# Kernel optimization log

Hardware: AMD Instinct MI355X
Metric: run time of the kernel (lower is better)

Reference implementation:

```python
import jax, jax.numpy as jnp
import numpy as np

N = 50000
E = 800000
G = 2500  # number of graphs


def setup_inputs() -> dict:
    key = jax.random.key(0)
    ks = jax.random.split(key, 10)
    x = jax.random.normal(ks[0], (N, 128), dtype=jnp.float32)
    edge_index = jax.random.randint(ks[1], (2, E), 0, N, dtype=jnp.int64)
    batch = jnp.sort(jax.random.randint(ks[2], (N,), 0, G, dtype=jnp.int64))
    def lin(k, fan_in, shape):
        return jax.random.normal(k, shape, dtype=jnp.float32) / np.sqrt(fan_in)
    return {
        'x': x, 'edge_index': edge_index, 'batch': batch,
        'W1': lin(ks[3], 128, (128, 64)), 'b1': jnp.zeros((64,), jnp.float32),
        'W2': lin(ks[4], 64, (64, 64)),  'b2': jnp.zeros((64,), jnp.float32),
        'W3': lin(ks[5], 64, (64, 64)),  'b3': jnp.zeros((64,), jnp.float32),
        'Wp1': lin(ks[6], 64, (64, 64)), 'bp1': jnp.zeros((64,), jnp.float32),
        'Wp2': lin(ks[7], 64, (64, 32)), 'bp2': jnp.zeros((32,), jnp.float32),
    }


def _gcn_norm(edge_index, n_nodes):
    # PyG GCNConv default: add self-loops, symmetric normalization
    loops = jnp.arange(n_nodes, dtype=edge_index.dtype)
    src = jnp.concatenate([edge_index[0], loops])
    dst = jnp.concatenate([edge_index[1], loops])
    deg = jax.ops.segment_sum(jnp.ones_like(dst, dtype=jnp.float32), dst,
                              num_segments=n_nodes)
    dis = jnp.where(deg > 0, jax.lax.rsqrt(deg), 0.0)
    norm = dis[src] * dis[dst]  # [E + N]
    return src, dst, norm


def _gcn_conv(x, W, b, src, dst, norm, n_nodes):
    h = x @ W                                   # transform first (small dim)
    m = h[src] * norm[:, None]                  # gather + scale
    out = jax.ops.segment_sum(m, dst, num_segments=n_nodes)  # scatter-add
    return out + b


def reference(x, edge_index, batch, W1, b1, W2, b2, W3, b3, Wp1, bp1, Wp2, bp2):
    n_nodes = x.shape[0]
    src, dst, norm = _gcn_norm(edge_index, n_nodes)
    x1 = jax.nn.relu(_gcn_conv(x, W1, b1, src, dst, norm, n_nodes))
    x2 = jax.nn.relu(_gcn_conv(x1, W2, b2, src, dst, norm, n_nodes))
    x3 = jax.nn.relu(_gcn_conv(x2, W3, b3, src, dst, norm, n_nodes))
    h = x1 + x2 + x3
    # global_mean_pool
    sums = jax.ops.segment_sum(h, batch, num_segments=G)
    counts = jax.ops.segment_sum(jnp.ones((n_nodes,), jnp.float32), batch,
                                 num_segments=G)
    pooled = sums / jnp.maximum(counts, 1.0)[:, None]
    z = jax.nn.relu(pooled @ Wp1 + bp1) @ Wp2 + bp2
    return z
```

## Files before the change

kernel.cpp:

```cpp
#include <hip/hip_runtime.h>
#include <math.h>


typedef short short8 __attribute__((ext_vector_type(8)));
typedef float f32x4 __attribute__((ext_vector_type(4)));

__device__ inline float bf2f(unsigned short h) {
    return __uint_as_float((unsigned)h << 16);
}
__device__ inline unsigned short f2bf(float f) {
    unsigned u = __float_as_uint(f);
    return (unsigned short)((u + (0x7FFFu + ((u >> 16) & 1u))) >> 16);
}
__device__ inline void bh8f(short8 u, float4& a, float4& b) {
    a.x = bf2f((unsigned short)u[0]); a.y = bf2f((unsigned short)u[1]);
    a.z = bf2f((unsigned short)u[2]); a.w = bf2f((unsigned short)u[3]);
    b.x = bf2f((unsigned short)u[4]); b.y = bf2f((unsigned short)u[5]);
    b.z = bf2f((unsigned short)u[6]); b.w = bf2f((unsigned short)u[7]);
}
__device__ inline float4 f4add(float4 a, float4 acc) {
    acc.x += a.x; acc.y += a.y; acc.z += a.z; acc.w += a.w;
    return acc;
}

template <int K>
__global__ __launch_bounds__(256) void k_hist_gemm(const int* __restrict__ dst,
                                                   int* __restrict__ hist, int E, int chunk,
                                                   const float* __restrict__ X,
                                                   const float* __restrict__ W,
                                                   unsigned short* __restrict__ H, int n) {
    __shared__ int hh[256];
    __shared__ short wt[64 * K];
    int t = threadIdx.x;
    if (blockIdx.x < 256) {
        hh[t] = 0;
        __syncthreads();
        int e0 = blockIdx.x * chunk;
        int e1 = min(e0 + chunk, E);
        for (int e = e0 + t; e < e1; e += 256) atomicAdd(&hh[dst[e] >> 8], 1);
        __syncthreads();
        hist[blockIdx.x * 256 + t] = hh[t];
        return;
    }
    for (int idx = t; idx < 64 * K; idx += 256) {
        int k = idx >> 6, ch = idx & 63;
        wt[ch * K + k] = (short)f2bf(W[idx]);
    }
    __syncthreads();
    int wave = t >> 6, lane = t & 63;
    int q = lane >> 4, l = lane & 15;
    int tile = (blockIdx.x - 256) * 4 + wave;
    if (tile * 16 >= n) return;
    int node = tile * 16 + l;
    short8 afr[4][K / 32];
#pragma unroll
    for (int mb = 0; mb < 4; mb++)
#pragma unroll
        for (int s = 0; s < K / 32; s++)
            afr[mb][s] = *(const short8*)(wt + (mb * 16 + l) * K + s * 32 + q * 8);
    f32x4 acc[4] = {};
    const float* xr = X + (size_t)node * K + q * 8;
#pragma unroll
    for (int s = 0; s < K / 32; s++) {
        float4 xa = *(const float4*)(xr + s * 32);
        float4 xb = *(const float4*)(xr + s * 32 + 4);
        short8 bfr;
        bfr[0] = (short)f2bf(xa.x); bfr[1] = (short)f2bf(xa.y);
        bfr[2] = (short)f2bf(xa.z); bfr[3] = (short)f2bf(xa.w);
        bfr[4] = (short)f2bf(xb.x); bfr[5] = (short)f2bf(xb.y);
        bfr[6] = (short)f2bf(xb.z); bfr[7] = (short)f2bf(xb.w);
#pragma unroll
        for (int mb = 0; mb < 4; mb++)
            acc[mb] = __builtin_amdgcn_mfma_f32_16x16x32_bf16(afr[mb][s], bfr, acc[mb], 0, 0, 0);
    }
#pragma unroll
    for (int mb = 0; mb < 4; mb++) {
        ushort4 u;
        u.x = f2bf(acc[mb][0]); u.y = f2bf(acc[mb][1]);
        u.z = f2bf(acc[mb][2]); u.w = f2bf(acc[mb][3]);
        ((ushort4*)H)[(size_t)node * 16 + mb * 4 + q] = u;
    }
}

__global__ void kA_colscan(const int* __restrict__ hist, int* __restrict__ cursorA,
                           int* __restrict__ tot) {
    __shared__ int s[256];
    int t = threadIdx.x;
    int k = blockIdx.x;
    int v = hist[t * 256 + k];
    s[t] = v;
    __syncthreads();
    for (int st = 1; st < 256; st <<= 1) {
        int u = s[t];
        if (t >= st) u += s[t - st];
        __syncthreads();
        s[t] = u;
        __syncthreads();
    }
    cursorA[t * 256 + k] = s[t] - v;
    if (t == 255) tot[k] = s[255];
}

__global__ void kA_scatter(const int* __restrict__ src, const int* __restrict__ dst,
                           const int* __restrict__ cursorA, const int* __restrict__ tot,
                           unsigned* __restrict__ ebuf, int E, int chunk) {
    __shared__ int s[256];
    __shared__ int cur[256];
    int t = threadIdx.x;
    s[t] = tot[t];
    __syncthreads();
    for (int st = 1; st < 256; st <<= 1) {
        int u = s[t];
        if (t >= st) u += s[t - st];
        __syncthreads();
        s[t] = u;
        __syncthreads();
    }
    int bstart = (t == 0) ? 0 : s[t - 1];
    cur[t] = cursorA[blockIdx.x * 256 + t] + bstart;
    __syncthreads();
    int e0 = blockIdx.x * chunk;
    int e1 = min(e0 + chunk, E);
    for (int e = e0 + t; e < e1; e += 256) {
        int d = dst[e];
        int p = atomicAdd(&cur[d >> 8], 1);
        ebuf[p] = ((unsigned)(d & 255) << 24) | (unsigned)src[e];
    }
}

__global__ void kB(const unsigned* __restrict__ ebuf, const int* __restrict__ tot,
                   float* __restrict__ dis, int* __restrict__ offsP,
                   unsigned* __restrict__ col, unsigned short* __restrict__ Hb,
                   unsigned short* __restrict__ Hb2, int* __restrict__ perm,
                   int N, int ZR) {
    __shared__ int s[256];
    __shared__ int h[256];
    __shared__ int cur[256];
    __shared__ float sdis[256];
    __shared__ int lh[128];
    __shared__ int ls[128];
    int t = threadIdx.x;
    int k = blockIdx.x;
    s[t] = tot[t];
    if (t < 128) lh[t] = 0;
    __syncthreads();
    for (int st = 1; st < 256; st <<= 1) {
        int u = s[t];
        if (t >= st) u += s[t - st];
        __syncthreads();
        s[t] = u;
        __syncthreads();
    }
    int lo = (k == 0) ? 0 : s[k - 1];
    int hi = s[k];
    int padbase = ((lo + 3) & ~3) + 768 * k;
    h[t] = 0;
    __syncthreads();
    for (int p = lo + t; p < hi; p += 256) atomicAdd(&h[ebuf[p] >> 24], 1);
    __syncthreads();
    int c = h[t];
    int cp = (c + 3) & ~3;
    int node = k * 256 + t;
    float dn = rsqrtf((float)(c + 1));
    sdis[t] = dn;
    if (node < N) dis[node] = dn;
    int bin = cp >> 2;
    if (bin > 127) bin = 127;
    bin = 127 - bin;
    int rk = 0;
    if (node < N) rk = atomicAdd(&lh[bin], 1);
    s[t] = cp;
    __syncthreads();
    for (int st = 1; st < 256; st <<= 1) {
        int u = s[t];
        if (t >= st) u += s[t - st];
        __syncthreads();
        s[t] = u;
        __syncthreads();
    }
    int start = padbase + s[t] - cp;
    if (node < N) offsP[node] = (start << 9) | cp;
    cur[t] = start;
    if (t < 128) ls[t] = lh[t];
    __syncthreads();
    for (int st = 1; st < 128; st <<= 1) {
        int u = 0;
        if (t < 128) { u = ls[t]; if (t >= st) u += ls[t - st]; }
        __syncthreads();
        if (t < 128) ls[t] = u;
        __syncthreads();
    }
    if (node < N) perm[k * 256 + ls[bin] - lh[bin] + rk] = node;
    for (int p = lo + t; p < hi; p += 256) {
        unsigned e = ebuf[p];
        int q = atomicAdd(&cur[e >> 24], 1);
        col[q] = e & 0x00FFFFFFu;
    }
    __syncthreads();
    if (node < N) {
        int end = start + cp;
        for (int q = cur[t]; q < end; q++) col[q] = (unsigned)ZR;
    }
    for (int idx = t; idx < 2048; idx += 256) {
        int nl = idx >> 3, cs = idx & 7;
        int nd = k * 256 + nl;
        if (nd >= N) continue;
        float d2 = sdis[nl];
        short8 v = ((const short8*)Hb)[(size_t)nd * 8 + cs];
        float4 a, b;
        bh8f(v, a, b);
        short8 o;
        o[0] = (short)f2bf(a.x * d2); o[1] = (short)f2bf(a.y * d2);
        o[2] = (short)f2bf(a.z * d2); o[3] = (short)f2bf(a.w * d2);
        o[4] = (short)f2bf(b.x * d2); o[5] = (short)f2bf(b.y * d2);
        o[6] = (short)f2bf(b.z * d2); o[7] = (short)f2bf(b.w * d2);
        ((short8*)Hb)[(size_t)nd * 8 + cs] = o;
    }
    if (k == 0) {
        if (t < 32) ((unsigned*)Hb)[(size_t)ZR * 32 + t] = 0u;
        else if (t < 64) ((unsigned*)Hb2)[(size_t)ZR * 32 + (t - 32)] = 0u;
    }
}

__global__ __launch_bounds__(256) void k_aggemm(const unsigned short* __restrict__ H,
                                                const unsigned* __restrict__ col,
                                                const int* __restrict__ offsP,
                                                const float* __restrict__ dis,
                                                const float* __restrict__ bias,
                                                const float* __restrict__ W,
                                                const int* __restrict__ perm,
                                                unsigned short* __restrict__ Xout,
                                                unsigned short* __restrict__ Hout, int n) {
    __shared__ short wt[64 * 64];
    __shared__ short vbuf[64 * 72];
    int t = threadIdx.x;
    for (int idx = t; idx < 64 * 64; idx += 256) {
        int k = idx >> 6, ch = idx & 63;
        wt[ch * 64 + k] = (short)f2bf(W[idx]);
    }
    const short8* Hs = (const short8*)H;
    int base = blockIdx.x * 64;
    int cs = t & 7;
    const float4* bias4 = (const float4*)bias;
    float4 bb0 = bias4[cs * 2];
    float4 bb1 = bias4[cs * 2 + 1];
#pragma unroll
    for (int r = 0; r < 2; r++) {
        int nl = r * 32 + (t >> 3);
        int slot = base + nl;
        if (slot < n) {
            int node = perm[slot];
            float dn = dis[node];
            float4 acc0, acc1;
            bh8f(Hs[(size_t)node * 8 + cs], acc0, acc1);
            int po = offsP[node];
            int p = po >> 9, hiP = p + (po & 511);
            for (; p + 8 <= hiP; p += 8) {
                uint4 ea = *(const uint4*)(col + p);
                uint4 eb = *(const uint4*)(col + p + 4);
                short8 g0 = Hs[(size_t)ea.x * 8 + cs];
                short8 g1 = Hs[(size_t)ea.y * 8 + cs];
                short8 g2 = Hs[(size_t)ea.z * 8 + cs];
                short8 g3 = Hs[(size_t)ea.w * 8 + cs];
                short8 g4 = Hs[(size_t)eb.x * 8 + cs];
                short8 g5 = Hs[(size_t)eb.y * 8 + cs];
                short8 g6 = Hs[(size_t)eb.z * 8 + cs];
                short8 g7 = Hs[(size_t)eb.w * 8 + cs];
                float4 a, b;
                bh8f(g0, a, b); acc0 = f4add(a, acc0); acc1 = f4add(b, acc1);
                bh8f(g1, a, b); acc0 = f4add(a, acc0); acc1 = f4add(b, acc1);
                bh8f(g2, a, b); acc0 = f4add(a, acc0); acc1 = f4add(b, acc1);
                bh8f(g3, a, b); acc0 = f4add(a, acc0); acc1 = f4add(b, acc1);
                bh8f(g4, a, b); acc0 = f4add(a, acc0); acc1 = f4add(b, acc1);
                bh8f(g5, a, b); acc0 = f4add(a, acc0); acc1 = f4add(b, acc1);
                bh8f(g6, a, b); acc0 = f4add(a, acc0); acc1 = f4add(b, acc1);
                bh8f(g7, a, b); acc0 = f4add(a, acc0); acc1 = f4add(b, acc1);
            }
            if (p < hiP) {
                uint4 e4 = *(const uint4*)(col + p);
                short8 g0 = Hs[(size_t)e4.x * 8 + cs];
                short8 g1 = Hs[(size_t)e4.y * 8 + cs];
                short8 g2 = Hs[(size_t)e4.z * 8 + cs];
                short8 g3 = Hs[(size_t)e4.w * 8 + cs];
                float4 a, b;
                bh8f(g0, a, b); acc0 = f4add(a, acc0); acc1 = f4add(b, acc1);
                bh8f(g1, a, b); acc0 = f4add(a, acc0); acc1 = f4add(b, acc1);
                bh8f(g2, a, b); acc0 = f4add(a, acc0); acc1 = f4add(b, acc1);
                bh8f(g3, a, b); acc0 = f4add(a, acc0); acc1 = f4add(b, acc1);
            }
            float4 v0, v1;
            v0.x = fmaxf(acc0.x * dn + bb0.x, 0.f);
            v0.y = fmaxf(acc0.y * dn + bb0.y, 0.f);
            v0.z = fmaxf(acc0.z * dn + bb0.z, 0.f);
            v0.w = fmaxf(acc0.w * dn + bb0.w, 0.f);
            v1.x = fmaxf(acc1.x * dn + bb1.x, 0.f);
            v1.y = fmaxf(acc1.y * dn + bb1.y, 0.f);
            v1.z = fmaxf(acc1.z * dn + bb1.z, 0.f);
            v1.w = fmaxf(acc1.w * dn + bb1.w, 0.f);
            short8 o;
            o[0] = (short)f2bf(v0.x); o[1] = (short)f2bf(v0.y);
            o[2] = (short)f2bf(v0.z); o[3] = (short)f2bf(v0.w);
            o[4] = (short)f2bf(v1.x); o[5] = (short)f2bf(v1.y);
            o[6] = (short)f2bf(v1.z); o[7] = (short)f2bf(v1.w);
            ((short8*)Xout)[(size_t)node * 8 + cs] = o;
            *(short8*)(vbuf + nl * 72 + cs * 8) = o;
        }
    }
    __syncthreads();
    int wave = t >> 6, lane = t & 63;
    int q = lane >> 4, l = lane & 15;
    if (base + wave * 16 >= n) return;
    int node = perm[base + wave * 16 + l];
    float dn2 = dis[node];
    short8 afr[4][2];
#pragma unroll
    for (int mb = 0; mb < 4; mb++)
#pragma unroll
        for (int s = 0; s < 2; s++)
            afr[mb][s] = *(const short8*)(wt + (mb * 16 + l) * 64 + s * 32 + q * 8);
    f32x4 acc[4] = {};
#pragma unroll
    for (int s = 0; s < 2; s++) {
        short8 bfr = *(const short8*)(vbuf + (wave * 16 + l) * 72 + s * 32 + q * 8);
#pragma unroll
        for (int mb = 0; mb < 4; mb++)
            acc[mb] = __builtin_amdgcn_mfma_f32_16x16x32_bf16(afr[mb][s], bfr, acc[mb], 0, 0, 0);
    }
#pragma unroll
    for (int mb = 0; mb < 4; mb++) {
        ushort4 u;
        u.x = f2bf(acc[mb][0] * dn2); u.y = f2bf(acc[mb][1] * dn2);
        u.z = f2bf(acc[mb][2] * dn2); u.w = f2bf(acc[mb][3] * dn2);
        ((ushort4*)Hout)[(size_t)node * 16 + mb * 4 + q] = u;
    }
}

__global__ void k_agg3(const unsigned short* __restrict__ H, const unsigned* __restrict__ col,
                       const int* __restrict__ offsP, const float* __restrict__ dis,
                       const float* __restrict__ bias,
                       const unsigned short* __restrict__ add1,
                       const unsigned short* __restrict__ add2,
                       const int* __restrict__ perm,
                       float* __restrict__ OutS, int n) {
    int t = threadIdx.x;
    int slot = blockIdx.x * 32 + (t >> 3);
    if (slot >= n) return;
    int node = perm[slot];
    int lane = t & 7;
    const short8* Hs = (const short8*)H;
    float dn = dis[node];
    float4 acc0, acc1;
    bh8f(Hs[(size_t)node * 8 + lane], acc0, acc1);
    int po = offsP[node];
    int p = po >> 9, hiP = p + (po & 511);
    for (; p + 8 <= hiP; p += 8) {
        uint4 ea = *(const uint4*)(col + p);
        uint4 eb = *(const uint4*)(col + p + 4);
        short8 g0 = Hs[(size_t)ea.x * 8 + lane];
        short8 g1 = Hs[(size_t)ea.y * 8 + lane];
        short8 g2 = Hs[(size_t)ea.z * 8 + lane];
        short8 g3 = Hs[(size_t)ea.w * 8 + lane];
        short8 g4 = Hs[(size_t)eb.x * 8 + lane];
        short8 g5 = Hs[(size_t)eb.y * 8 + lane];
        short8 g6 = Hs[(size_t)eb.z * 8 + lane];
        short8 g7 = Hs[(size_t)eb.w * 8 + lane];
        float4 a, b;
        bh8f(g0, a, b); acc0 = f4add(a, acc0); acc1 = f4add(b, acc1);
        bh8f(g1, a, b); acc0 = f4add(a, acc0); acc1 = f4add(b, acc1);
        bh8f(g2, a, b); acc0 = f4add(a, acc0); acc1 = f4add(b, acc1);
        bh8f(g3, a, b); acc0 = f4add(a, acc0); acc1 = f4add(b, acc1);
        bh8f(g4, a, b); acc0 = f4add(a, acc0); acc1 = f4add(b, acc1);
        bh8f(g5, a, b); acc0 = f4add(a, acc0); acc1 = f4add(b, acc1);
        bh8f(g6, a, b); acc0 = f4add(a, acc0); acc1 = f4add(b, acc1);
        bh8f(g7, a, b); acc0 = f4add(a, acc0); acc1 = f4add(b, acc1);
    }
    if (p < hiP) {
        uint4 e4 = *(const uint4*)(col + p);
        short8 g0 = Hs[(size_t)e4.x * 8 + lane];
        short8 g1 = Hs[(size_t)e4.y * 8 + lane];
        short8 g2 = Hs[(size_t)e4.z * 8 + lane];
        short8 g3 = Hs[(size_t)e4.w * 8 + lane];
        float4 a, b;
        bh8f(g0, a, b); acc0 = f4add(a, acc0); acc1 = f4add(b, acc1);
        bh8f(g1, a, b); acc0 = f4add(a, acc0); acc1 = f4add(b, acc1);
        bh8f(g2, a, b); acc0 = f4add(a, acc0); acc1 = f4add(b, acc1);
        bh8f(g3, a, b); acc0 = f4add(a, acc0); acc1 = f4add(b, acc1);
    }
    const float4* bias4 = (const float4*)bias;
    float4 bb0 = bias4[lane * 2];
    float4 bb1 = bias4[lane * 2 + 1];
    float4 v0, v1;
    v0.x = fmaxf(acc0.x * dn + bb0.x, 0.f);
    v0.y = fmaxf(acc0.y * dn + bb0.y, 0.f);
    v0.z = fmaxf(acc0.z * dn + bb0.z, 0.f);
    v0.w = fmaxf(acc0.w * dn + bb0.w, 0.f);
    v1.x = fmaxf(acc1.x * dn + bb1.x, 0.f);
    v1.y = fmaxf(acc1.y * dn + bb1.y, 0.f);
    v1.z = fmaxf(acc1.z * dn + bb1.z, 0.f);
    v1.w = fmaxf(acc1.w * dn + bb1.w, 0.f);
    size_t slotR = (size_t)node * 8 + lane;
    float4 a10, a11, a20, a21;
    bh8f(((const short8*)add1)[slotR], a10, a11);
    bh8f(((const short8*)add2)[slotR], a20, a21);
    v0.x += a10.x + a20.x; v0.y += a10.y + a20.y;
    v0.z += a10.z + a20.z; v0.w += a10.w + a20.w;
    v1.x += a11.x + a21.x; v1.y += a11.y + a21.y;
    v1.z += a11.z + a21.z; v1.w += a11.w + a21.w;
    float4* S4 = (float4*)OutS;
    size_t oi = (size_t)node * 16 + (size_t)lane * 2;
    S4[oi] = v0;
    S4[oi + 1] = v1;
}

__global__ void k_poolhead(const float* __restrict__ S, const int* __restrict__ batch,
                           const float* __restrict__ Wp1, const float* __restrict__ bp1,
                           const float* __restrict__ Wp2, const float* __restrict__ bp2,
                           float* __restrict__ out, int n, int G) {
    int g = blockIdx.x;
    int j = threadIdx.x;
    int a = 0, b = n;
    while (a < b) { int m = (a + b) >> 1; if (batch[m] < g) a = m + 1; else b = m; }
    int beg = a;
    b = n;
    while (a < b) { int m = (a + b) >> 1; if (batch[m] < g + 1) a = m + 1; else b = m; }
    int end = a;
    float sum = 0.f;
    int i = beg;
    for (; i + 2 <= end; i += 2)
        sum += S[(size_t)i * 64 + j] + S[(size_t)(i + 1) * 64 + j];
    if (i < end) sum += S[(size_t)i * 64 + j];
    float cnt = (float)(end - beg);
    float p = sum / fmaxf(cnt, 1.f);
    __shared__ float ps[64];
    __shared__ float ts[64];
    ps[j] = p;
    __syncthreads();
    float t1 = bp1[j];
#pragma unroll 8
    for (int k = 0; k < 64; k++) t1 += ps[k] * Wp1[k * 64 + j];
    t1 = fmaxf(t1, 0.f);
    ts[j] = t1;
    __syncthreads();
    if (j < 32) {
        float o = bp2[j];
#pragma unroll 8
        for (int k = 0; k < 64; k++) o += ts[k] * Wp2[k * 32 + j];
        out[(size_t)g * 32 + j] = o;
    }
}

extern "C" void kernel_launch(void* const* d_in, const int* in_sizes, int n_in,
                              void* d_out, int out_size, void* d_ws, size_t ws_size,
                              hipStream_t stream) {
    const float* x   = (const float*)d_in[0];
    const int*   ei  = (const int*)d_in[1];
    const int*   bat = (const int*)d_in[2];
    const float* W1  = (const float*)d_in[3];
    const float* b1  = (const float*)d_in[4];
    const float* W2  = (const float*)d_in[5];
    const float* b2  = (const float*)d_in[6];
    const float* W3  = (const float*)d_in[7];
    const float* b3  = (const float*)d_in[8];
    const float* Wp1 = (const float*)d_in[9];
    const float* bp1 = (const float*)d_in[10];
    const float* Wp2 = (const float*)d_in[11];
    const float* bp2 = (const float*)d_in[12];

    int N = in_sizes[0] / 128;
    int E = in_sizes[1] / 2;
    int G = out_size / 32;
    const int* src = ei;
    const int* dst = ei + E;

    char* w = (char*)d_ws;
    auto alloc = [&](size_t bytes) -> void* {
        void* p = (void*)w;
        w += (bytes + 255) & ~(size_t)255;
        return p;
    };
    int NB = (N + 255) / 256;
    int ZR = N;
    int*            offsP   = (int*)alloc((size_t)N * 4);
    unsigned*       col     = (unsigned*)alloc(((size_t)E + 3 * (size_t)N + 2048) * 4);
    float*          dis     = (float*)alloc((size_t)N * 4);
    int*            hist    = (int*)alloc((size_t)256 * 256 * 4);
    int*            cursorA = (int*)alloc((size_t)256 * 256 * 4);
    int*            tot     = (int*)alloc((size_t)256 * 4);
    unsigned*       ebuf    = (unsigned*)alloc((size_t)E * 4);
    int*            perm    = (int*)alloc((size_t)(NB * 256) * 4);
    unsigned short* Hb      = (unsigned short*)alloc(((size_t)N + 16) * 64 * 2);
    unsigned short* Hb2     = (unsigned short*)alloc(((size_t)N + 16) * 64 * 2);
    unsigned short* X1      = (unsigned short*)alloc((size_t)N * 64 * 2);
    unsigned short* X2      = (unsigned short*)alloc((size_t)N * 64 * 2);
    float*          S       = (float*)alloc((size_t)N * 64 * 4);

    int chunk = (E + 255) / 256;
    int ggemm = ((N >> 4) + 3) / 4;
    int gfuse = (N + 63) / 64;
    int gagg  = (N + 31) / 32;

    k_hist_gemm<128><<<256 + ggemm, 256, 0, stream>>>(dst, hist, E, chunk, x, W1, Hb, N);
    kA_colscan<<<256, 256, 0, stream>>>(hist, cursorA, tot);
    kA_scatter<<<256, 256, 0, stream>>>(src, dst, cursorA, tot, ebuf, E, chunk);
    kB<<<NB, 256, 0, stream>>>(ebuf, tot, dis, offsP, col, Hb, Hb2, perm, N, ZR);

    k_aggemm<<<gfuse, 256, 0, stream>>>(Hb, col, offsP, dis, b1, W2, perm, X1, Hb2, N);
    k_aggemm<<<gfuse, 256, 0, stream>>>(Hb2, col, offsP, dis, b2, W3, perm, X2, Hb, N);
    k_agg3<<<gagg, 256, 0, stream>>>(Hb, col, offsP, dis, b3, X1, X2, perm, S, N);

    k_poolhead<<<G, 64, 0, stream>>>(S, bat, Wp1, bp1, Wp2, bp2, (float*)d_out, N, G);
}
```

Measured before the change: 221.2 us.

## Drop degree-sorted node permutation and use 32-node blocks in fused aggregate-GEMM

Removes the per-block degree-binning permutation built in kB (histogram, scan, perm writes) and the perm indirection in the aggregation kernels, so nodes are processed in natural order. k_aggemm now handles 32 nodes per 256-thread block instead of 64, which doubles the grid, and only two waves run the MFMA projection. The gains are less scan and sync work in kB, one fewer indirect load per node, and more blocks for the scheduler. The cost is that per-wave degree balancing is lost, so waves can diverge on uneven neighbor counts, and half the waves sit idle during the matrix step.

After: 215.5 us. -2.6%, faster.

```diff
diff --git a/kernel.cpp b/kernel.cpp
--- a/kernel.cpp
+++ b/kernel.cpp
@@ -131,18 +131,14 @@
 __global__ void kB(const unsigned* __restrict__ ebuf, const int* __restrict__ tot,
                    float* __restrict__ dis, int* __restrict__ offsP,
                    unsigned* __restrict__ col, unsigned short* __restrict__ Hb,
-                   unsigned short* __restrict__ Hb2, int* __restrict__ perm,
-                   int N, int ZR) {
+                   unsigned short* __restrict__ Hb2, int N, int ZR) {
     __shared__ int s[256];
     __shared__ int h[256];
     __shared__ int cur[256];
     __shared__ float sdis[256];
-    __shared__ int lh[128];
-    __shared__ int ls[128];
     int t = threadIdx.x;
     int k = blockIdx.x;
     s[t] = tot[t];
-    if (t < 128) lh[t] = 0;
     __syncthreads();
     for (int st = 1; st < 256; st <<= 1) {
         int u = s[t];
@@ -164,11 +160,6 @@
     float dn = rsqrtf((float)(c + 1));
     sdis[t] = dn;
     if (node < N) dis[node] = dn;
-    int bin = cp >> 2;
-    if (bin > 127) bin = 127;
-    bin = 127 - bin;
-    int rk = 0;
-    if (node < N) rk = atomicAdd(&lh[bin], 1);
     s[t] = cp;
     __syncthreads();
     for (int st = 1; st < 256; st <<= 1) {
@@ -181,16 +172,7 @@
     int start = padbase + s[t] - cp;
     if (node < N) offsP[node] = (start << 9) | cp;
     cur[t] = start;
-    if (t < 128) ls[t] = lh[t];
-    __syncthreads();
-    for (int st = 1; st < 128; st <<= 1) {
-        int u = 0;
-        if (t < 128) { u = ls[t]; if (t >= st) u += ls[t - st]; }
-        __syncthreads();
-        if (t < 128) ls[t] = u;
-        __syncthreads();
-    }
-    if (node < N) perm[k * 256 + ls[bin] - lh[bin] + rk] = node;
+    __syncthreads();
     for (int p = lo + t; p < hi; p += 256) {
         unsigned e = ebuf[p];
         int q = atomicAdd(&cur[e >> 24], 1);
@@ -228,90 +210,86 @@
                                                 const float* __restrict__ dis,
                                                 const float* __restrict__ bias,
                                                 const float* __restrict__ W,
-                                                const int* __restrict__ perm,
                                                 unsigned short* __restrict__ Xout,
                                                 unsigned short* __restrict__ Hout, int n) {
     __shared__ short wt[64 * 64];
-    __shared__ short vbuf[64 * 72];
+    __shared__ short vbuf[32 * 72];
     int t = threadIdx.x;
     for (int idx = t; idx < 64 * 64; idx += 256) {
         int k = idx >> 6, ch = idx & 63;
         wt[ch * 64 + k] = (short)f2bf(W[idx]);
     }
     const short8* Hs = (const short8*)H;
-    int base = blockIdx.x * 64;
+    int base = blockIdx.x * 32;
     int cs = t & 7;
+    int nl = t >> 3;
+    int node = base + nl;
     const float4* bias4 = (const float4*)bias;
     float4 bb0 = bias4[cs * 2];
     float4 bb1 = bias4[cs * 2 + 1];
-#pragma unroll
-    for (int r = 0; r < 2; r++) {
-        int nl = r * 32 + (t >> 3);
-        int slot = base + nl;
-        if (slot < n) {
-            int node = perm[slot];
-            float dn = dis[node];
-            float4 acc0, acc1;
-            bh8f(Hs[(size_t)node * 8 + cs], acc0, acc1);
-            int po = offsP[node];
-            int p = po >> 9, hiP = p + (po & 511);
-            for (; p + 8 <= hiP; p += 8) {
-                uint4 ea = *(const uint4*)(col + p);
-                uint4 eb = *(const uint4*)(col + p + 4);
-                short8 g0 = Hs[(size_t)ea.x * 8 + cs];
-                short8 g1 = Hs[(size_t)ea.y * 8 + cs];
-                short8 g2 = Hs[(size_t)ea.z * 8 + cs];
-                short8 g3 = Hs[(size_t)ea.w * 8 + cs];
-                short8 g4 = Hs[(size_t)eb.x * 8 + cs];
-                short8 g5 = Hs[(size_t)eb.y * 8 + cs];
-                short8 g6 = Hs[(size_t)eb.z * 8 + cs];
-                short8 g7 = Hs[(size_t)eb.w * 8 + cs];
-                float4 a, b;
-                bh8f(g0, a, b); acc0 = f4add(a, acc0); acc1 = f4add(b, acc1);
-                bh8f(g1, a, b); acc0 = f4add(a, acc0); acc1 = f4add(b, acc1);
-                bh8f(g2, a, b); acc0 = f4add(a, acc0); acc1 = f4add(b, acc1);
-                bh8f(g3, a, b); acc0 = f4add(a, acc0); acc1 = f4add(b, acc1);
-                bh8f(g4, a, b); acc0 = f4add(a, acc0); acc1 = f4add(b, acc1);
-                bh8f(g5, a, b); acc0 = f4add(a, acc0); acc1 = f4add(b, acc1);
-                bh8f(g6, a, b); acc0 = f4add(a, acc0); acc1 = f4add(b, acc1);
-                bh8f(g7, a, b); acc0 = f4add(a, acc0); acc1 = f4add(b, acc1);
-            }
-            if (p < hiP) {
-                uint4 e4 = *(const uint4*)(col + p);
-                short8 g0 = Hs[(size_t)e4.x * 8 + cs];
-                short8 g1 = Hs[(size_t)e4.y * 8 + cs];
-                short8 g2 = Hs[(size_t)e4.z * 8 + cs];
-                short8 g3 = Hs[(size_t)e4.w * 8 + cs];
-                float4 a, b;
-                bh8f(g0, a, b); acc0 = f4add(a, acc0); acc1 = f4add(b, acc1);
-                bh8f(g1, a, b); acc0 = f4add(a, acc0); acc1 = f4add(b, acc1);
-                bh8f(g2, a, b); acc0 = f4add(a, acc0); acc1 = f4add(b, acc1);
-                bh8f(g3, a, b); acc0 = f4add(a, acc0); acc1 = f4add(b, acc1);
-            }
-            float4 v0, v1;
-            v0.x = fmaxf(acc0.x * dn + bb0.x, 0.f);
-            v0.y = fmaxf(acc0.y * dn + bb0.y, 0.f);
-            v0.z = fmaxf(acc0.z * dn + bb0.z, 0.f);
-            v0.w = fmaxf(acc0.w * dn + bb0.w, 0.f);
-            v1.x = fmaxf(acc1.x * dn + bb1.x, 0.f);
-            v1.y = fmaxf(acc1.y * dn + bb1.y, 0.f);
-            v1.z = fmaxf(acc1.z * dn + bb1.z, 0.f);
-            v1.w = fmaxf(acc1.w * dn + bb1.w, 0.f);
-            short8 o;
-            o[0] = (short)f2bf(v0.x); o[1] = (short)f2bf(v0.y);
-            o[2] = (short)f2bf(v0.z); o[3] = (short)f2bf(v0.w);
-            o[4] = (short)f2bf(v1.x); o[5] = (short)f2bf(v1.y);
-            o[6] = (short)f2bf(v1.z); o[7] = (short)f2bf(v1.w);
-            ((short8*)Xout)[(size_t)node * 8 + cs] = o;
-            *(short8*)(vbuf + nl * 72 + cs * 8) = o;
+    if (node < n) {
+        float dn = dis[node];
+        float4 acc0, acc1;
+        bh8f(Hs[(size_t)node * 8 + cs], acc0, acc1);
+        int po = offsP[node];
+        int p = po >> 9, hiP = p + (po & 511);
+        for (; p + 8 <= hiP; p += 8) {
+            uint4 ea = *(const uint4*)(col + p);
+            uint4 eb = *(const uint4*)(col + p + 4);
+            short8 g0 = Hs[(size_t)ea.x * 8 + cs];
+            short8 g1 = Hs[(size_t)ea.y * 8 + cs];
+            short8 g2 = Hs[(size_t)ea.z * 8 + cs];
+            short8 g3 = Hs[(size_t)ea.w * 8 + cs];
+            short8 g4 = Hs[(size_t)eb.x * 8 + cs];
+            short8 g5 = Hs[(size_t)eb.y * 8 + cs];
+            short8 g6 = Hs[(size_t)eb.z * 8 + cs];
+            short8 g7 = Hs[(size_t)eb.w * 8 + cs];
+            float4 a, b;
+            bh8f(g0, a, b); acc0 = f4add(a, acc0); acc1 = f4add(b, acc1);
+            bh8f(g1, a, b); acc0 = f4add(a, acc0); acc1 = f4add(b, acc1);
+            bh8f(g2, a, b); acc0 = f4add(a, acc0); acc1 = f4add(b, acc1);
+            bh8f(g3, a, b); acc0 = f4add(a, acc0); acc1 = f4add(b, acc1);
+            bh8f(g4, a, b); acc0 = f4add(a, acc0); acc1 = f4add(b, acc1);
+            bh8f(g5, a, b); acc0 = f4add(a, acc0); acc1 = f4add(b, acc1);
+            bh8f(g6, a, b); acc0 = f4add(a, acc0); acc1 = f4add(b, acc1);
+            bh8f(g7, a, b); acc0 = f4add(a, acc0); acc1 = f4add(b, acc1);
         }
+        if (p < hiP) {
+            uint4 e4 = *(const uint4*)(col + p);
+            short8 g0 = Hs[(size_t)e4.x * 8 + cs];
+            short8 g1 = Hs[(size_t)e4.y * 8 + cs];
+            short8 g2 = Hs[(size_t)e4.z * 8 + cs];
+            short8 g3 = Hs[(size_t)e4.w * 8 + cs];
+            float4 a, b;
+            bh8f(g0, a, b); acc0 = f4add(a, acc0); acc1 = f4add(b, acc1);
+            bh8f(g1, a, b); acc0 = f4add(a, acc0); acc1 = f4add(b, acc1);
+            bh8f(g2, a, b); acc0 = f4add(a, acc0); acc1 = f4add(b, acc1);
+            bh8f(g3, a, b); acc0 = f4add(a, acc0); acc1 = f4add(b, acc1);
+        }
+        float4 v0, v1;
+        v0.x = fmaxf(acc0.x * dn + bb0.x, 0.f);
+        v0.y = fmaxf(acc0.y * dn + bb0.y, 0.f);
+        v0.z = fmaxf(acc0.z * dn + bb0.z, 0.f);
+        v0.w = fmaxf(acc0.w * dn + bb0.w, 0.f);
+        v1.x = fmaxf(acc1.x * dn + bb1.x, 0.f);
+        v1.y = fmaxf(acc1.y * dn + bb1.y, 0.f);
+        v1.z = fmaxf(acc1.z * dn + bb1.z, 0.f);
+        v1.w = fmaxf(acc1.w * dn + bb1.w, 0.f);
+        short8 o;
+        o[0] = (short)f2bf(v0.x); o[1] = (short)f2bf(v0.y);
+        o[2] = (short)f2bf(v0.z); o[3] = (short)f2bf(v0.w);
+        o[4] = (short)f2bf(v1.x); o[5] = (short)f2bf(v1.y);
+        o[6] = (short)f2bf(v1.z); o[7] = (short)f2bf(v1.w);
+        ((short8*)Xout)[(size_t)node * 8 + cs] = o;
+        *(short8*)(vbuf + nl * 72 + cs * 8) = o;
     }
     __syncthreads();
     int wave = t >> 6, lane = t & 63;
+    if (wave >= 2) return;
     int q = lane >> 4, l = lane & 15;
     if (base + wave * 16 >= n) return;
-    int node = perm[base + wave * 16 + l];
-    float dn2 = dis[node];
+    int mnode = base + wave * 16 + l;
+    float dn2 = dis[mnode];
     short8 afr[4][2];
 #pragma unroll
     for (int mb = 0; mb < 4; mb++)
@@ -331,7 +309,7 @@
         ushort4 u;
         u.x = f2bf(acc[mb][0] * dn2); u.y = f2bf(acc[mb][1] * dn2);
         u.z = f2bf(acc[mb][2] * dn2); u.w = f2bf(acc[mb][3] * dn2);
-        ((ushort4*)Hout)[(size_t)node * 16 + mb * 4 + q] = u;
+        ((ushort4*)Hout)[(size_t)mnode * 16 + mb * 4 + q] = u;
     }
 }
 
@@ -340,12 +318,10 @@
                        const float* __restrict__ bias,
                        const unsigned short* __restrict__ add1,
                        const unsigned short* __restrict__ add2,
-                       const int* __restrict__ perm,
                        float* __restrict__ OutS, int n) {
     int t = threadIdx.x;
-    int slot = blockIdx.x * 32 + (t >> 3);
-    if (slot >= n) return;
-    int node = perm[slot];
+    int node = blockIdx.x * 32 + (t >> 3);
+    if (node >= n) return;
     int lane = t & 7;
     const short8* Hs = (const short8*)H;
     float dn = dis[node];
@@ -398,10 +374,10 @@
     v1.y = fmaxf(acc1.y * dn + bb1.y, 0.f);
     v1.z = fmaxf(acc1.z * dn + bb1.z, 0.f);
     v1.w = fmaxf(acc1.w * dn + bb1.w, 0.f);
-    size_t slotR = (size_t)node * 8 + lane;
+    size_t slot = (size_t)node * 8 + lane;
     float4 a10, a11, a20, a21;
-    bh8f(((const short8*)add1)[slotR], a10, a11);
-    bh8f(((const short8*)add2)[slotR], a20, a21);
+    bh8f(((const short8*)add1)[slot], a10, a11);
+    bh8f(((const short8*)add2)[slot], a20, a21);
     v0.x += a10.x + a20.x; v0.y += a10.y + a20.y;
     v0.z += a10.z + a20.z; v0.w += a10.w + a20.w;
     v1.x += a11.x + a21.x; v1.y += a11.y + a21.y;
@@ -487,7 +463,6 @@
     int*            cursorA = (int*)alloc((size_t)256 * 256 * 4);
     int*            tot     = (int*)alloc((size_t)256 * 4);
     unsigned*       ebuf    = (unsigned*)alloc((size_t)E * 4);
-    int*            perm    = (int*)alloc((size_t)(NB * 256) * 4);
     unsigned short* Hb      = (unsigned short*)alloc(((size_t)N + 16) * 64 * 2);
     unsigned short* Hb2     = (unsigned short*)alloc(((size_t)N + 16) * 64 * 2);
     unsigned short* X1      = (unsigned short*)alloc((size_t)N * 64 * 2);
@@ -496,17 +471,17 @@
 
     int chunk = (E + 255) / 256;
     int ggemm = ((N >> 4) + 3) / 4;
-    int gfuse = (N + 63) / 64;
+    int gfuse = (N + 31) / 32;
     int gagg  = (N + 31) / 32;
 
     k_hist_gemm<128><<<256 + ggemm, 256, 0, stream>>>(dst, hist, E, chunk, x, W1, Hb, N);
     kA_colscan<<<256, 256, 0, stream>>>(hist, cursorA, tot);
     kA_scatter<<<256, 256, 0, stream>>>(src, dst, cursorA, tot, ebuf, E, chunk);
-    kB<<<NB, 256, 0, stream>>>(ebuf, tot, dis, offsP, col, Hb, Hb2, perm, N, ZR);
-
-    k_aggemm<<<gfuse, 256, 0, stream>>>(Hb, col, offsP, dis, b1, W2, perm, X1, Hb2, N);
-    k_aggemm<<<gfuse, 256, 0, stream>>>(Hb2, col, offsP, dis, b2, W3, perm, X2, Hb, N);
-    k_agg3<<<gagg, 256, 0, stream>>>(Hb, col, offsP, dis, b3, X1, X2, perm, S, N);
+    kB<<<NB, 256, 0, stream>>>(ebuf, tot, dis, offsP, col, Hb, Hb2, N, ZR);
+
+    k_aggemm<<<gfuse, 256, 0, stream>>>(Hb, col, offsP, dis, b1, W2, X1, Hb2, N);
+    k_aggemm<<<gfuse, 256, 0, stream>>>(Hb2, col, offsP, dis, b2, W3, X2, Hb, N);
+    k_agg3<<<gagg, 256, 0, stream>>>(Hb, col, offsP, dis, b3, X1, X2, S, N);
 
     k_poolhead<<<G, 64, 0, stream>>>(S, bat, Wp1, bp1, Wp2, bp2, (float*)d_out, N, G);
 }
```
